# Optimization experiments

Hardware: AMD Instinct MI355X
Metric: run time of the kernel (lower is better)

The kernel has to match this reference:

```python
import jax, jax.numpy as jnp
import numpy as np

NSAMPLE = 64
RADIUS = 0.3
HMIN = -0.2
HMAX_LIST = (0.1, 0.2, 0.3, 0.4)
NUM_ANGLE = 12
NUM_DEPTH = 4
EPS = 1e-5


def setup_inputs() -> dict:
    key = jax.random.key(0)
    ks = jax.random.split(key, 32)
    rn = lambda i, s: jax.random.normal(ks[i], s, dtype=jnp.float32)
    ru = lambda i, s: jax.random.uniform(ks[i], s, dtype=jnp.float32)
    return {
        'seed_xyz': rn(0, (2, 1024, 3)),
        'pointcloud': rn(1, (2, 8192, 3)),
        'vp_rot': rn(2, (2, 1024, 3, 3)),
        'cw1': rn(3, (64, 3)), 'cbn1': ru(4, (4, 64)),
        'cw2': rn(5, (128, 64)), 'cbn2': ru(6, (4, 128)),
        'cw3': rn(7, (256, 128)), 'cbn3': ru(8, (4, 256)),
        'ow1': rn(9, (128, 256)), 'ob1': rn(10, (128,)), 'obn1': ru(11, (4, 128)),
        'ow2': rn(12, (128, 128)), 'ob2': rn(13, (128,)), 'obn2': ru(14, (4, 128)),
        'ow3': rn(15, (36, 128)), 'ob3': rn(16, (36,)),
        'tw1': rn(17, (128, 256)), 'tb1': rn(18, (128,)), 'tbn1': ru(19, (4, 128)),
        'tw2': rn(20, (128, 128)), 'tb2': rn(21, (128,)), 'tbn2': ru(22, (4, 128)),
        'tw3': rn(23, (12, 128)), 'tb3': rn(24, (12,)),
    }


def _bn_relu(y, bn):
    g, b, m, v = bn[0], bn[1], bn[2], bn[3]
    return jax.nn.relu(g * (y - m) * jax.lax.rsqrt(v + EPS) + b)


def _bn(y, bn):
    g, b, m, v = bn[0], bn[1], bn[2], bn[3]
    return g * (y - m) * jax.lax.rsqrt(v + EPS) + b


def _forward(seed_xyz, pointcloud, vp_rot, cw1, cbn1, cw2, cbn2, cw3, cbn3,
             ow1, ob1, obn1, ow2, ob2, obn2, ow3, ob3,
             tw1, tb1, tbn1, tw2, tb2, tbn2, tw3, tb3):
    B, ns, _ = seed_xyz.shape
    N = pointcloud.shape[1]
    # relative coords of every scene point w.r.t. every seed, rotated into the
    # grasp-view frame (cylinder axis = x after rotation): (B, ns, N, 3)
    rel = pointcloud[:, None, :, :] - seed_xyz[:, :, None, :]
    rot_rel = jnp.einsum('bsnc,bscd->bsnd', rel, vp_rot)
    ax = rot_rel[..., 0]
    r2 = rot_rel[..., 1] ** 2 + rot_rel[..., 2] ** 2
    pref = jnp.arange(N, dtype=jnp.float32) / N  # earlier index preferred (CUDA scan order)
    groups = []
    for hmax in HMAX_LIST:
        mask = (ax > HMIN) & (ax < hmax) & (r2 < RADIUS * RADIUS)
        score = mask.astype(jnp.float32) * 2.0 - pref
        _, idx = jax.lax.top_k(score, NSAMPLE)  # (B, ns, NSAMPLE), first valid idxs in order
        valid = jnp.take_along_axis(mask, idx, axis=-1)
        idx = jnp.where(valid, idx, idx[..., :1])  # fill slots with first found index
        g = jnp.take_along_axis(rot_rel, idx[..., None], axis=2)  # (B, ns, NSAMPLE, 3)
        groups.append(g)
    feat = jnp.stack(groups, axis=2)  # (B, ns, num_depth, NSAMPLE, 3)
    feat = feat.reshape(B, ns * NUM_DEPTH, NSAMPLE, 3)
    # SharedMLP [3,64,128,256], conv2d 1x1 (no bias) + BN + ReLU
    h = _bn_relu(feat @ cw1.T, cbn1)
    h = _bn_relu(h @ cw2.T, cbn2)
    h = _bn_relu(h @ cw3.T, cbn3)
    vp = jnp.max(h, axis=2)  # max-pool over nsample -> (B, ns*num_depth, 256)

    def head(w1, b1, bn1, w2, b2, bn2, w3, b3):
        x = _bn_relu(vp @ w1.T + b1, bn1)
        x = _bn_relu(x @ w2.T + b2, bn2)
        return x @ w3.T + b3

    op = head(ow1, ob1, obn1, ow2, ob2, obn2, ow3, ob3)     # (B, ns*D, 3*num_angle)
    tol = head(tw1, tb1, tbn1, tw2, tb2, tbn2, tw3, tb3)    # (B, ns*D, num_angle)
    out = jnp.concatenate([op, tol], axis=-1)               # score|angle_cls|width|tolerance
    out = out.reshape(B, ns, NUM_DEPTH, 4 * NUM_ANGLE).transpose(0, 3, 1, 2)
    return out  # (B, 4*num_angle, num_seed, num_depth)


def reference(seed_xyz, pointcloud, vp_rot, cw1, cbn1, cw2, cbn2, cw3, cbn3,
              ow1, ob1, obn1, ow2, ob2, obn2, ow3, ob3,
              tw1, tb1, tbn1, tw2, tb2, tbn2, tw3, tb3):
    return _forward(seed_xyz, pointcloud, vp_rot, cw1, cbn1, cw2, cbn2, cw3, cbn3,
                    ow1, ob1, obn1, ow2, ob2, obn2, ow3, ob3,
                    tw1, tb1, tbn1, tw2, tb2, tbn2, tw3, tb3)
```

## Files before the change

### kernel.cpp

```cpp
#include <hip/hip_runtime.h>
#include <hip/hip_bf16.h>

#define NB    2
#define NS    1024
#define NPTS  8192
#define NGROUP (NB*NS*4)

enum : int {
  OFF_BW2  = 256,
  OFF_W1Q  = 4352,
  OFF_B2   = 8448,
  OFF_BW3  = 8576,
  OFF_B3   = 41344,
  OFF_HB1  = 41600,
  OFF_HB1B = 74368,
  OFF_HB2  = 74624,
  OFF_HB2B = 107392,
  OFF_HB3  = 107648,
  OFF_HB3B = 115840,
  PREP_TOTAL = 189632,
  OFF_FEAT = 146688,
  OFF_VP   = 1719552,
  OFF_CNT  = 3816704,
  OFF_FLAG = 3824896,
};

struct Ptrs { const void* p[25]; };

typedef __attribute__((ext_vector_type(8))) short bf16x8;
typedef __attribute__((ext_vector_type(4))) float f32x4;

template<typename T> struct LD;
template<> struct LD<float> {
  static __device__ __forceinline__ float get(const void* p, int i){ return ((const float*)p)[i]; }
};
template<> struct LD<__hip_bfloat16> {
  static __device__ __forceinline__ float get(const void* p, int i){ return __bfloat162float(((const __hip_bfloat16*)p)[i]); }
};

template<typename T>
__device__ __forceinline__ float bnscale(const void* bn, int C, int c){
  float g = LD<T>::get(bn, c);
  float v = LD<T>::get(bn, 3*C + c);
  return g / sqrtf(v + 1e-5f);
}

__device__ __forceinline__ unsigned short f2bf(float v){
  __hip_bfloat16 hb = __float2bfloat16(v);
  return *reinterpret_cast<unsigned short*>(&hb);
}

__global__ __launch_bounds__(256) void detect_kernel(const void* w2, const void* w3, int* flag){
  __shared__ int f;
  int t = threadIdx.x;
  if (t == 0) f = 0;
  __syncthreads();
  int loc = 0;
  const unsigned short* a = (const unsigned short*)w2;
  for (int i = t; i < 8192; i += 256)  loc |= ((a[i] & 0x7F80) == 0x7F80);
  const unsigned short* b = (const unsigned short*)w3;
  for (int i = t; i < 32768; i += 256) loc |= ((b[i] & 0x7F80) == 0x7F80);
  if (loc) atomicOr(&f, 1);
  __syncthreads();
  if (t == 0) flag[0] = f;
}

template<typename T>
__global__ __launch_bounds__(256) void prep_kernel(Ptrs in, float* __restrict__ ws, int want){
  if (((const volatile int*)(ws + OFF_FLAG))[0] != want) return;
  int i = blockIdx.x*256 + threadIdx.x;
  if (i >= PREP_TOTAL) return;
  if (i < 256) { int c = i>>2, d = i&3; float s = bnscale<T>(in.p[4],64,c);
    float v = (d<3) ? LD<T>::get(in.p[3], c*3+d)*s
                    : LD<T>::get(in.p[4],64+c) - LD<T>::get(in.p[4],2*64+c)*s;
    ws[OFF_W1Q+i] = v; return; }
  i -= 256;
  if (i < 8192) {
    int j = i&7, f = i>>3, lane = f&63, kn = f>>6, kt = kn&1, nt = kn>>1;
    int n = nt*16 + (lane&15), k = kt*32 + ((lane>>4)<<3) + j;
    float s = bnscale<T>(in.p[6],128,n);
    ((unsigned short*)(ws + OFF_BW2))[i] = f2bf(LD<T>::get(in.p[5], n*64+k)*s); return; }
  i -= 8192;
  if (i < 32768) {
    int j = i&7, f = i>>3, lane = f&63, kn = f>>6, kt = kn&3, nt = kn>>2;
    int n = nt*16 + (lane&15), k = kt*32 + ((lane>>4)<<3) + j;
    float s = bnscale<T>(in.p[8],256,n);
    ((unsigned short*)(ws + OFF_BW3))[i] = f2bf(LD<T>::get(in.p[7], n*128+k)*s); return; }
  i -= 32768;
  if (i < 128) { float s = bnscale<T>(in.p[6],128,i);
    ws[OFF_B2+i] = LD<T>::get(in.p[6],128+i) - LD<T>::get(in.p[6],2*128+i)*s; return; }
  i -= 128;
  if (i < 256) { float s = bnscale<T>(in.p[8],256,i);
    ws[OFF_B3+i] = LD<T>::get(in.p[8],256+i) - LD<T>::get(in.p[8],2*256+i)*s; return; }
  i -= 256;
  if (i < 65536) {
    int j = i&7, f = i>>3, lane = f&63, kn = f>>6, kt = kn&7, nt = kn>>3;
    int n = nt*16 + (lane&15), k = kt*32 + ((lane>>4)<<3) + j;
    float v;
    if (n < 128) v = LD<T>::get(in.p[9],  n*256+k)       * bnscale<T>(in.p[11],128,n);
    else         v = LD<T>::get(in.p[17], (n-128)*256+k) * bnscale<T>(in.p[19],128,n-128);
    ((unsigned short*)(ws + OFF_HB1))[i] = f2bf(v); return; }
  i -= 65536;
  if (i < 256) { int n = i; float v;
    if (n < 128) { float s = bnscale<T>(in.p[11],128,n);
      v = (LD<T>::get(in.p[10],n) - LD<T>::get(in.p[11],2*128+n))*s + LD<T>::get(in.p[11],128+n); }
    else { int m = n-128; float s = bnscale<T>(in.p[19],128,m);
      v = (LD<T>::get(in.p[18],m) - LD<T>::get(in.p[19],2*128+m))*s + LD<T>::get(in.p[19],128+m); }
    ws[OFF_HB1B+n] = v; return; }
  i -= 256;
  if (i < 65536) {
    int j = i&7, f = i>>3, lane = f&63, kn = f>>6, kt = kn&7, nt = kn>>3;
    int n = nt*16 + (lane&15), k = kt*32 + ((lane>>4)<<3) + j;
    float v = 0.f;
    if (n < 128) { if (k < 128)  v = LD<T>::get(in.p[12], n*128+k)            * bnscale<T>(in.p[14],128,n); }
    else         { if (k >= 128) v = LD<T>::get(in.p[20], (n-128)*128+(k-128)) * bnscale<T>(in.p[22],128,n-128); }
    ((unsigned short*)(ws + OFF_HB2))[i] = f2bf(v); return; }
  i -= 65536;
  if (i < 256) { int n = i; float v;
    if (n < 128) { float s = bnscale<T>(in.p[14],128,n);
      v = (LD<T>::get(in.p[13],n) - LD<T>::get(in.p[14],2*128+n))*s + LD<T>::get(in.p[14],128+n); }
    else { int m = n-128; float s = bnscale<T>(in.p[22],128,m);
      v = (LD<T>::get(in.p[21],m) - LD<T>::get(in.p[22],2*128+m))*s + LD<T>::get(in.p[22],128+m); }
    ws[OFF_HB2B+n] = v; return; }
  i -= 256;
  if (i < 16384) {
    int j = i&7, f = i>>3, lane = f&63, kn = f>>6, kt = kn&7, nt = kn>>3;
    int n = nt*16 + (lane&15), k = kt*32 + ((lane>>4)<<3) + j;
    float v = 0.f;
    if (n < 36)      { if (k < 128)  v = LD<T>::get(in.p[15], n*128+k); }
    else if (n < 48) { if (k >= 128) v = LD<T>::get(in.p[23], (n-36)*128+(k-128)); }
    ((unsigned short*)(ws + OFF_HB3))[i] = f2bf(v); return; }
  i -= 16384;
  { int n = i; float v = 0.f;
    if (n < 36) v = LD<T>::get(in.p[16], n);
    else if (n < 48) v = LD<T>::get(in.p[24], n-36);
    ws[OFF_HB3B+n] = v; }
}

template<typename T>
__global__ __launch_bounds__(256) void group_kernel(
    const void* __restrict__ seed, const void* __restrict__ pc,
    const void* __restrict__ vr, float* __restrict__ ws, int want)
{
#pragma clang fp contract(off)
  if (((const volatile int*)(ws + OFF_FLAG))[0] != want) return;
  float* feat = ws + OFF_FEAT;
  int* cnt = (int*)(ws + OFF_CNT);
  __shared__ float rxs[256], rys[256], rzs[256];
  int bs = blockIdx.x;
  int b = bs >> 10;
  int t = threadIdx.x;
  int wave = t >> 6, lane = t & 63;
  float sx = LD<T>::get(seed, bs*3+0), sy = LD<T>::get(seed, bs*3+1), sz = LD<T>::get(seed, bs*3+2);
  float r00=LD<T>::get(vr,bs*9+0), r01=LD<T>::get(vr,bs*9+1), r02=LD<T>::get(vr,bs*9+2);
  float r10=LD<T>::get(vr,bs*9+3), r11=LD<T>::get(vr,bs*9+4), r12=LD<T>::get(vr,bs*9+5);
  float r20=LD<T>::get(vr,bs*9+6), r21=LD<T>::get(vr,bs*9+7), r22=LD<T>::get(vr,bs*9+8);
  const float hmaxs[4] = {0.1f, 0.2f, 0.3f, 0.4f};
  float hmax = hmaxs[wave];
  int g = bs*4 + wave;
  float* fout = feat + g*192;
  int base = b*(NPTS*3);
  int count = 0;
  float p0x=0.f, p0y=0.f, p0z=0.f;
  for (int c0 = 0; c0 < NPTS; c0 += 256) {
    __syncthreads();
    { int pi = base + (c0 + t)*3;
      float e0 = LD<T>::get(pc, pi+0) - sx;
      float e1 = LD<T>::get(pc, pi+1) - sy;
      float e2 = LD<T>::get(pc, pi+2) - sz;
      rxs[t] = e0*r00 + e1*r10 + e2*r20;
      rys[t] = e0*r01 + e1*r11 + e2*r21;
      rzs[t] = e0*r02 + e1*r12 + e2*r22; }
    __syncthreads();
    if (count < 64) {
      for (int sub = 0; sub < 4; ++sub) {
        int idx = sub*64 + lane;
        float rx = rxs[idx], ry = rys[idx], rz = rzs[idx];
        float r2 = ry*ry + rz*rz;
        bool m = (rx > -0.2f) && (rx < hmax) && (r2 < 0.09f);
        unsigned long long bal = __ballot(m);
        int rank = __popcll(bal & ((1ull << lane) - 1ull));
        int slot = count + rank;
        if (m && slot < 64) { fout[slot*3+0]=rx; fout[slot*3+1]=ry; fout[slot*3+2]=rz; }
        count += __popcll(bal);
      }
    }
    if (c0 == 0) { p0x = rxs[0]; p0y = rys[0]; p0z = rzs[0]; }
  }
  if (count == 0) {
    if (lane == 0) { fout[0]=p0x; fout[1]=p0y; fout[2]=p0z; }
    count = 1;
  }
  if (lane == 0) cnt[g] = (count > 64) ? 64 : count;
}

__global__ __launch_bounds__(256) void mlp_kernel(float* __restrict__ ws){
  __shared__ unsigned short h2s[2][64*136];
  __shared__ float w1q[4][256];
  const int t = threadIdx.x;
  const int wave = t >> 6, lane = t & 63;
  const int quad = lane >> 4, l15 = lane & 15;
  const int grp = wave >> 1, nhalf = wave & 1;
  const int g = blockIdx.x*2 + grp;
  for (int i = t; i < 1024; i += 256) w1q[i>>8][i&255] = ws[OFF_W1Q + (i&255)];
  const int V = ((const int*)(ws + OFF_CNT))[g];
  const float* feat = ws + OFF_FEAT + g*192;
  __syncthreads();
  bf16x8 a1[4][2];
  const float* wq = w1q[quad];
#pragma unroll
  for (int mt = 0; mt < 4; ++mt) {
    const int m = mt*16 + l15;
    const float x0 = feat[m*3+0], x1 = feat[m*3+1], x2 = feat[m*3+2];
#pragma unroll
    for (int kt = 0; kt < 2; ++kt) {
      const int c0 = kt*32 + quad*8;
#pragma unroll
      for (int j = 0; j < 8; ++j) {
        const float* w = wq + (c0+j)*4;
        a1[mt][kt][j] = (short)f2bf(fmaxf(w[3] + x0*w[0] + x1*w[1] + x2*w[2], 0.f));
      }
    }
  }
  unsigned short* h2 = h2s[grp];
  const bf16x8* BW2 = (const bf16x8*)(ws + OFF_BW2);
#pragma unroll
  for (int nt4 = 0; nt4 < 4; ++nt4) {
    const int nt = nhalf*4 + nt4;
    const int n = nt*16 + l15;
    const float bias = ws[OFF_B2 + n];
    f32x4 acc[4];
#pragma unroll
    for (int mt = 0; mt < 4; ++mt) acc[mt] = (f32x4){bias, bias, bias, bias};
#pragma unroll
    for (int kt = 0; kt < 2; ++kt) {
      const bf16x8 b = BW2[(nt*2+kt)*64 + lane];
#pragma unroll
      for (int mt = 0; mt < 4; ++mt)
        acc[mt] = __builtin_amdgcn_mfma_f32_16x16x32_bf16(a1[mt][kt], b, acc[mt], 0, 0, 0);
    }
#pragma unroll
    for (int mt = 0; mt < 4; ++mt)
#pragma unroll
      for (int jj = 0; jj < 4; ++jj) {
        const int m = mt*16 + quad*4 + jj;
        h2[m*136 + n] = f2bf(fmaxf(acc[mt][jj], 0.f));
      }
  }
  __syncthreads();
  bf16x8 a2[4][4];
#pragma unroll
  for (int mt = 0; mt < 4; ++mt)
#pragma unroll
    for (int kt = 0; kt < 4; ++kt)
      a2[mt][kt] = *(const bf16x8*)&h2[(mt*16 + l15)*136 + kt*32 + quad*8];
  const bf16x8* BW3 = (const bf16x8*)(ws + OFF_BW3);
  float vpv[8];
#pragma unroll
  for (int nt8 = 0; nt8 < 8; ++nt8) {
    const int nt = nhalf*8 + nt8;
    const int n = nt*16 + l15;
    const float bias = ws[OFF_B3 + n];
    f32x4 acc[4];
#pragma unroll
    for (int mt = 0; mt < 4; ++mt) acc[mt] = (f32x4){bias, bias, bias, bias};
#pragma unroll
    for (int kt = 0; kt < 4; ++kt) {
      const bf16x8 b = BW3[(nt*4+kt)*64 + lane];
#pragma unroll
      for (int mt = 0; mt < 4; ++mt)
        acc[mt] = __builtin_amdgcn_mfma_f32_16x16x32_bf16(a2[mt][kt], b, acc[mt], 0, 0, 0);
    }
    float mx = 0.f;
#pragma unroll
    for (int mt = 0; mt < 4; ++mt)
#pragma unroll
      for (int jj = 0; jj < 4; ++jj) {
        const int row = mt*16 + quad*4 + jj;
        const float v = fmaxf(acc[mt][jj], 0.f);
        mx = (row < V) ? fmaxf(mx, v) : mx;
      }
    mx = fmaxf(mx, __shfl_xor(mx, 16, 64));
    mx = fmaxf(mx, __shfl_xor(mx, 32, 64));
    vpv[nt8] = mx;
  }
  if (quad == 0) {
    float* vp = ws + OFF_VP + g*256 + nhalf*128;
#pragma unroll
    for (int nt8 = 0; nt8 < 8; ++nt8) vp[nt8*16 + l15] = vpv[nt8];
  }
}

#define YSTRIDE 264
template<typename OUT>
__global__ __launch_bounds__(256) void heads_kernel(float* __restrict__ ws, OUT* __restrict__ out, int want){
  if (((const volatile int*)(ws + OFF_FLAG))[0] != want) return;
  __shared__ unsigned short y[16*YSTRIDE];
  const int t = threadIdx.x;
  const int wave = t >> 6, lane = t & 63;
  const int quad = lane >> 4, l15 = lane & 15;
  const int r0 = blockIdx.x * 16;
  bf16x8 a[8];
  const float* vp = ws + OFF_VP + (r0 + l15)*256;
#pragma unroll
  for (int kt = 0; kt < 8; ++kt) {
    const float4* v4 = (const float4*)(vp + kt*32 + quad*8);
    float4 u0 = v4[0], u1 = v4[1];
    a[kt][0]=(short)f2bf(u0.x); a[kt][1]=(short)f2bf(u0.y); a[kt][2]=(short)f2bf(u0.z); a[kt][3]=(short)f2bf(u0.w);
    a[kt][4]=(short)f2bf(u1.x); a[kt][5]=(short)f2bf(u1.y); a[kt][6]=(short)f2bf(u1.z); a[kt][7]=(short)f2bf(u1.w);
  }
  const bf16x8* HB1 = (const bf16x8*)(ws + OFF_HB1);
#pragma unroll
  for (int nt4 = 0; nt4 < 4; ++nt4) {
    const int nt = wave*4 + nt4;
    const int n = nt*16 + l15;
    const float bias = ws[OFF_HB1B + n];
    f32x4 acc = (f32x4){bias, bias, bias, bias};
#pragma unroll
    for (int kt = 0; kt < 8; ++kt)
      acc = __builtin_amdgcn_mfma_f32_16x16x32_bf16(a[kt], HB1[(nt*8+kt)*64 + lane], acc, 0, 0, 0);
#pragma unroll
    for (int jj = 0; jj < 4; ++jj)
      y[(quad*4+jj)*YSTRIDE + n] = f2bf(fmaxf(acc[jj], 0.f));
  }
  __syncthreads();
#pragma unroll
  for (int kt = 0; kt < 8; ++kt)
    a[kt] = *(const bf16x8*)&y[l15*YSTRIDE + kt*32 + quad*8];
  __syncthreads();
  const bf16x8* HB2 = (const bf16x8*)(ws + OFF_HB2);
#pragma unroll
  for (int nt4 = 0; nt4 < 4; ++nt4) {
    const int nt = wave*4 + nt4;
    const int n = nt*16 + l15;
    const float bias = ws[OFF_HB2B + n];
    f32x4 acc = (f32x4){bias, bias, bias, bias};
#pragma unroll
    for (int kt = 0; kt < 8; ++kt)
      acc = __builtin_amdgcn_mfma_f32_16x16x32_bf16(a[kt], HB2[(nt*8+kt)*64 + lane], acc, 0, 0, 0);
#pragma unroll
    for (int jj = 0; jj < 4; ++jj)
      y[(quad*4+jj)*YSTRIDE + n] = f2bf(fmaxf(acc[jj], 0.f));
  }
  __syncthreads();
#pragma unroll
  for (int kt = 0; kt < 8; ++kt)
    a[kt] = *(const bf16x8*)&y[l15*YSTRIDE + kt*32 + quad*8];
  const bf16x8* HB3 = (const bf16x8*)(ws + OFF_HB3);
  {
    const int n = wave*16 + l15;
    const float bias = ws[OFF_HB3B + n];
    f32x4 acc = (f32x4){bias, bias, bias, bias};
#pragma unroll
    for (int kt = 0; kt < 8; ++kt)
      acc = __builtin_amdgcn_mfma_f32_16x16x32_bf16(a[kt], HB3[(wave*8+kt)*64 + lane], acc, 0, 0, 0);
    if (n < 48) {
#pragma unroll
      for (int jj = 0; jj < 4; ++jj) {
        const int gr = r0 + quad*4 + jj;
        const int b = gr >> 12, rem = gr & 4095, s = rem >> 2, d = rem & 3;
        out[((b*48 + n)*1024 + s)*4 + d] = (OUT)acc[jj];
      }
    }
  }
}

extern "C" void kernel_launch(void* const* d_in, const int* in_sizes, int n_in,
                              void* d_out, int out_size, void* d_ws, size_t ws_size,
                              hipStream_t stream) {
  float* ws = (float*)d_ws;
  Ptrs P;
  for (int i = 0; i < 25; ++i) P.p[i] = d_in[i];
  detect_kernel<<<1, 256, 0, stream>>>(d_in[5], d_in[7], (int*)(ws + OFF_FLAG));
  prep_kernel<__hip_bfloat16><<<(PREP_TOTAL+255)/256, 256, 0, stream>>>(P, ws, 0);
  prep_kernel<float><<<(PREP_TOTAL+255)/256, 256, 0, stream>>>(P, ws, 1);
  group_kernel<__hip_bfloat16><<<NB*NS, 256, 0, stream>>>(d_in[0], d_in[1], d_in[2], ws, 0);
  group_kernel<float><<<NB*NS, 256, 0, stream>>>(d_in[0], d_in[1], d_in[2], ws, 1);
  mlp_kernel<<<NGROUP/2, 256, 0, stream>>>(ws);
  heads_kernel<__hip_bfloat16><<<NGROUP/16, 256, 0, stream>>>(ws, (__hip_bfloat16*)d_out, 0);
  heads_kernel<float><<<NGROUP/16, 256, 0, stream>>>(ws, (float*)d_out, 1);
}
```

Before: 240.4 us.

## Double-buffer point staging, prefilter empty waves, skip empty MFMA row tiles

The grouping kernel now double-buffers the rotated point coordinates in shared memory, so staging the next chunk overlaps with scanning the current one and one barrier per iteration is removed. While staging, each wave also ballots a loose mask using the widest height bound, so scanning waves can skip 64-point sub-chunks that hold no candidates. The MLP kernel skips MFMA row tiles beyond the valid sample count, avoiding matrix work on padding rows. These add branches inside unrolled loops, which may raise register pressure or cause divergence-related code bloat, and the double buffer doubles the shared-memory footprint.

```diff
diff --git a/kernel.cpp b/kernel.cpp
--- a/kernel.cpp
+++ b/kernel.cpp
@@ -146,7 +146,8 @@
   if (((const volatile int*)(ws + OFF_FLAG))[0] != want) return;
   float* feat = ws + OFF_FEAT;
   int* cnt = (int*)(ws + OFF_CNT);
-  __shared__ float rxs[256], rys[256], rzs[256];
+  __shared__ float rxs[2][256], rys[2][256], rzs[2][256];
+  __shared__ unsigned long long loose[2][4];
   int bs = blockIdx.x;
   int b = bs >> 10;
   int t = threadIdx.x;
@@ -162,20 +163,34 @@
   int base = b*(NPTS*3);
   int count = 0;
   float p0x=0.f, p0y=0.f, p0z=0.f;
-  for (int c0 = 0; c0 < NPTS; c0 += 256) {
+
+  auto stage = [&](int c0, int buf){
+    int pi = base + (c0 + t)*3;
+    float e0 = LD<T>::get(pc, pi+0) - sx;
+    float e1 = LD<T>::get(pc, pi+1) - sy;
+    float e2 = LD<T>::get(pc, pi+2) - sz;
+    float rx = e0*r00 + e1*r10 + e2*r20;
+    float ry = e0*r01 + e1*r11 + e2*r21;
+    float rz = e0*r02 + e1*r12 + e2*r22;
+    rxs[buf][t] = rx; rys[buf][t] = ry; rzs[buf][t] = rz;
+    float r2 = ry*ry + rz*rz;
+    bool lm = (rx > -0.2f) && (rx < 0.4f) && (r2 < 0.09f);
+    unsigned long long bal = __ballot(lm);
+    if (lane == 0) loose[buf][wave] = bal;
+  };
+
+  stage(0, 0);
+  for (int c = 0; c < NPTS/256; ++c) {
+    int buf = c & 1;
     __syncthreads();
-    { int pi = base + (c0 + t)*3;
-      float e0 = LD<T>::get(pc, pi+0) - sx;
-      float e1 = LD<T>::get(pc, pi+1) - sy;
-      float e2 = LD<T>::get(pc, pi+2) - sz;
-      rxs[t] = e0*r00 + e1*r10 + e2*r20;
-      rys[t] = e0*r01 + e1*r11 + e2*r21;
-      rzs[t] = e0*r02 + e1*r12 + e2*r22; }
-    __syncthreads();
+    if (c == 0) { p0x = rxs[0][0]; p0y = rys[0][0]; p0z = rzs[0][0]; }
+    if (c + 1 < NPTS/256) stage((c+1)*256, 1 - buf);
     if (count < 64) {
       for (int sub = 0; sub < 4; ++sub) {
+        unsigned long long lb = loose[buf][sub];
+        if (lb == 0ull) continue;
         int idx = sub*64 + lane;
-        float rx = rxs[idx], ry = rys[idx], rz = rzs[idx];
+        float rx = rxs[buf][idx], ry = rys[buf][idx], rz = rzs[buf][idx];
         float r2 = ry*ry + rz*rz;
         bool m = (rx > -0.2f) && (rx < hmax) && (r2 < 0.09f);
         unsigned long long bal = __ballot(m);
@@ -185,7 +200,6 @@
         count += __popcll(bal);
       }
     }
-    if (c0 == 0) { p0x = rxs[0]; p0y = rys[0]; p0z = rzs[0]; }
   }
   if (count == 0) {
     if (lane == 0) { fout[0]=p0x; fout[1]=p0y; fout[2]=p0z; }
@@ -204,12 +218,13 @@
   const int g = blockIdx.x*2 + grp;
   for (int i = t; i < 1024; i += 256) w1q[i>>8][i&255] = ws[OFF_W1Q + (i&255)];
   const int V = ((const int*)(ws + OFF_CNT))[g];
+  const int MT = (V + 15) >> 4;
   const float* feat = ws + OFF_FEAT + g*192;
   __syncthreads();
   bf16x8 a1[4][2];
   const float* wq = w1q[quad];
 #pragma unroll
-  for (int mt = 0; mt < 4; ++mt) {
+  for (int mt = 0; mt < 4; ++mt) if (mt < MT) {
     const int m = mt*16 + l15;
     const float x0 = feat[m*3+0], x1 = feat[m*3+1], x2 = feat[m*3+2];
 #pragma unroll
@@ -231,16 +246,16 @@
     const float bias = ws[OFF_B2 + n];
     f32x4 acc[4];
 #pragma unroll
-    for (int mt = 0; mt < 4; ++mt) acc[mt] = (f32x4){bias, bias, bias, bias};
+    for (int mt = 0; mt < 4; ++mt) if (mt < MT) acc[mt] = (f32x4){bias, bias, bias, bias};
 #pragma unroll
     for (int kt = 0; kt < 2; ++kt) {
       const bf16x8 b = BW2[(nt*2+kt)*64 + lane];
 #pragma unroll
-      for (int mt = 0; mt < 4; ++mt)
+      for (int mt = 0; mt < 4; ++mt) if (mt < MT)
         acc[mt] = __builtin_amdgcn_mfma_f32_16x16x32_bf16(a1[mt][kt], b, acc[mt], 0, 0, 0);
     }
 #pragma unroll
-    for (int mt = 0; mt < 4; ++mt)
+    for (int mt = 0; mt < 4; ++mt) if (mt < MT)
 #pragma unroll
       for (int jj = 0; jj < 4; ++jj) {
         const int m = mt*16 + quad*4 + jj;
@@ -250,7 +265,7 @@
   __syncthreads();
   bf16x8 a2[4][4];
 #pragma unroll
-  for (int mt = 0; mt < 4; ++mt)
+  for (int mt = 0; mt < 4; ++mt) if (mt < MT)
 #pragma unroll
     for (int kt = 0; kt < 4; ++kt)
       a2[mt][kt] = *(const bf16x8*)&h2[(mt*16 + l15)*136 + kt*32 + quad*8];
@@ -263,17 +278,17 @@
     const float bias = ws[OFF_B3 + n];
     f32x4 acc[4];
 #pragma unroll
-    for (int mt = 0; mt < 4; ++mt) acc[mt] = (f32x4){bias, bias, bias, bias};
+    for (int mt = 0; mt < 4; ++mt) if (mt < MT) acc[mt] = (f32x4){bias, bias, bias, bias};
 #pragma unroll
     for (int kt = 0; kt < 4; ++kt) {
       const bf16x8 b = BW3[(nt*4+kt)*64 + lane];
 #pragma unroll
-      for (int mt = 0; mt < 4; ++mt)
+      for (int mt = 0; mt < 4; ++mt) if (mt < MT)
         acc[mt] = __builtin_amdgcn_mfma_f32_16x16x32_bf16(a2[mt][kt], b, acc[mt], 0, 0, 0);
     }
     float mx = 0.f;
 #pragma unroll
-    for (int mt = 0; mt < 4; ++mt)
+    for (int mt = 0; mt < 4; ++mt) if (mt < MT)
 #pragma unroll
       for (int jj = 0; jj < 4; ++jj) {
         const int row = mt*16 + quad*4 + jj;
```

Result: slower. 356.9 us (+48.5%).

## Restructure grouping to one wave per seed over all heights and merge dtype launches

Applied to the files above, without the earlier changes.

The grouping kernel now gives each wave a whole seed and classifies every point against all four height thresholds in one pass. Before, each block handled one seed, staged rotated points in shared memory, and used a wave per threshold. This removes the shared-memory staging and block barriers and computes each point's rotation once instead of four times. Waves can no longer stop early per threshold and must scan all 8192 points. The dtype-specific duplicate launches of prep, group and heads are merged into single launches that branch on the flag at runtime, cutting empty kernel launches.

```diff
diff --git a/kernel.cpp b/kernel.cpp
--- a/kernel.cpp
+++ b/kernel.cpp
@@ -66,10 +66,7 @@
 }
 
 template<typename T>
-__global__ __launch_bounds__(256) void prep_kernel(Ptrs in, float* __restrict__ ws, int want){
-  if (((const volatile int*)(ws + OFF_FLAG))[0] != want) return;
-  int i = blockIdx.x*256 + threadIdx.x;
-  if (i >= PREP_TOTAL) return;
+__device__ void prep_body(const Ptrs& in, float* __restrict__ ws, int i){
   if (i < 256) { int c = i>>2, d = i&3; float s = bnscale<T>(in.p[4],64,c);
     float v = (d<3) ? LD<T>::get(in.p[3], c*3+d)*s
                     : LD<T>::get(in.p[4],64+c) - LD<T>::get(in.p[4],2*64+c)*s;
@@ -137,61 +134,80 @@
     ws[OFF_HB3B+n] = v; }
 }
 
+__global__ __launch_bounds__(256) void prep_kernel(Ptrs in, float* __restrict__ ws){
+  int i = blockIdx.x*256 + threadIdx.x;
+  if (i >= PREP_TOTAL) return;
+  if (((const volatile int*)(ws + OFF_FLAG))[0]) prep_body<float>(in, ws, i);
+  else                                           prep_body<__hip_bfloat16>(in, ws, i);
+}
+
 template<typename T>
-__global__ __launch_bounds__(256) void group_kernel(
-    const void* __restrict__ seed, const void* __restrict__ pc,
-    const void* __restrict__ vr, float* __restrict__ ws, int want)
-{
+__device__ void group_body(const void* __restrict__ seed, const void* __restrict__ pc,
+                           float* __restrict__ ws, const void* __restrict__ vr, int bs){
 #pragma clang fp contract(off)
-  if (((const volatile int*)(ws + OFF_FLAG))[0] != want) return;
   float* feat = ws + OFF_FEAT;
   int* cnt = (int*)(ws + OFF_CNT);
-  __shared__ float rxs[256], rys[256], rzs[256];
-  int bs = blockIdx.x;
-  int b = bs >> 10;
-  int t = threadIdx.x;
-  int wave = t >> 6, lane = t & 63;
+  const int lane = threadIdx.x & 63;
+  const int b = bs >> 10;
   float sx = LD<T>::get(seed, bs*3+0), sy = LD<T>::get(seed, bs*3+1), sz = LD<T>::get(seed, bs*3+2);
   float r00=LD<T>::get(vr,bs*9+0), r01=LD<T>::get(vr,bs*9+1), r02=LD<T>::get(vr,bs*9+2);
   float r10=LD<T>::get(vr,bs*9+3), r11=LD<T>::get(vr,bs*9+4), r12=LD<T>::get(vr,bs*9+5);
   float r20=LD<T>::get(vr,bs*9+6), r21=LD<T>::get(vr,bs*9+7), r22=LD<T>::get(vr,bs*9+8);
-  const float hmaxs[4] = {0.1f, 0.2f, 0.3f, 0.4f};
-  float hmax = hmaxs[wave];
-  int g = bs*4 + wave;
-  float* fout = feat + g*192;
-  int base = b*(NPTS*3);
-  int count = 0;
+  float* f0 = feat + (bs*4+0)*192;
+  float* f1 = feat + (bs*4+1)*192;
+  float* f2 = feat + (bs*4+2)*192;
+  float* f3 = feat + (bs*4+3)*192;
+  int c0n=0, c1n=0, c2n=0, c3n=0;
+  const int base = b*(NPTS*3);
   float p0x=0.f, p0y=0.f, p0z=0.f;
-  for (int c0 = 0; c0 < NPTS; c0 += 256) {
-    __syncthreads();
-    { int pi = base + (c0 + t)*3;
-      float e0 = LD<T>::get(pc, pi+0) - sx;
-      float e1 = LD<T>::get(pc, pi+1) - sy;
-      float e2 = LD<T>::get(pc, pi+2) - sz;
-      rxs[t] = e0*r00 + e1*r10 + e2*r20;
-      rys[t] = e0*r01 + e1*r11 + e2*r21;
-      rzs[t] = e0*r02 + e1*r12 + e2*r22; }
-    __syncthreads();
-    if (count < 64) {
-      for (int sub = 0; sub < 4; ++sub) {
-        int idx = sub*64 + lane;
-        float rx = rxs[idx], ry = rys[idx], rz = rzs[idx];
-        float r2 = ry*ry + rz*rz;
-        bool m = (rx > -0.2f) && (rx < hmax) && (r2 < 0.09f);
-        unsigned long long bal = __ballot(m);
-        int rank = __popcll(bal & ((1ull << lane) - 1ull));
-        int slot = count + rank;
-        if (m && slot < 64) { fout[slot*3+0]=rx; fout[slot*3+1]=ry; fout[slot*3+2]=rz; }
-        count += __popcll(bal);
-      }
-    }
-    if (c0 == 0) { p0x = rxs[0]; p0y = rys[0]; p0z = rzs[0]; }
-  }
-  if (count == 0) {
-    if (lane == 0) { fout[0]=p0x; fout[1]=p0y; fout[2]=p0z; }
-    count = 1;
-  }
-  if (lane == 0) cnt[g] = (count > 64) ? 64 : count;
+  for (int c = 0; c < NPTS/64; ++c) {
+    const int pi = base + (c*64 + lane)*3;
+    float e0 = LD<T>::get(pc, pi+0) - sx;
+    float e1 = LD<T>::get(pc, pi+1) - sy;
+    float e2 = LD<T>::get(pc, pi+2) - sz;
+    float rx = e0*r00 + e1*r10 + e2*r20;
+    float ry = e0*r01 + e1*r11 + e2*r21;
+    float rz = e0*r02 + e1*r12 + e2*r22;
+    float r2 = ry*ry + rz*rz;
+    if (c == 0 && lane == 0) { p0x = rx; p0y = ry; p0z = rz; }
+    const bool mb = (rx > -0.2f) && (r2 < 0.09f);
+    const unsigned long long pm = (1ull << lane) - 1ull;
+    { bool m = mb && (rx < 0.1f); unsigned long long bal = __ballot(m);
+      if (bal) { int slot = c0n + __popcll(bal & pm);
+        if (m && slot < 64) { f0[slot*3]=rx; f0[slot*3+1]=ry; f0[slot*3+2]=rz; }
+        c0n += __popcll(bal); } }
+    { bool m = mb && (rx < 0.2f); unsigned long long bal = __ballot(m);
+      if (bal) { int slot = c1n + __popcll(bal & pm);
+        if (m && slot < 64) { f1[slot*3]=rx; f1[slot*3+1]=ry; f1[slot*3+2]=rz; }
+        c1n += __popcll(bal); } }
+    { bool m = mb && (rx < 0.3f); unsigned long long bal = __ballot(m);
+      if (bal) { int slot = c2n + __popcll(bal & pm);
+        if (m && slot < 64) { f2[slot*3]=rx; f2[slot*3+1]=ry; f2[slot*3+2]=rz; }
+        c2n += __popcll(bal); } }
+    { bool m = mb && (rx < 0.4f); unsigned long long bal = __ballot(m);
+      if (bal) { int slot = c3n + __popcll(bal & pm);
+        if (m && slot < 64) { f3[slot*3]=rx; f3[slot*3+1]=ry; f3[slot*3+2]=rz; }
+        c3n += __popcll(bal); } }
+  }
+  if (lane == 0) {
+    if (c0n == 0) { f0[0]=p0x; f0[1]=p0y; f0[2]=p0z; c0n = 1; }
+    if (c1n == 0) { f1[0]=p0x; f1[1]=p0y; f1[2]=p0z; c1n = 1; }
+    if (c2n == 0) { f2[0]=p0x; f2[1]=p0y; f2[2]=p0z; c2n = 1; }
+    if (c3n == 0) { f3[0]=p0x; f3[1]=p0y; f3[2]=p0z; c3n = 1; }
+    cnt[bs*4+0] = (c0n > 64) ? 64 : c0n;
+    cnt[bs*4+1] = (c1n > 64) ? 64 : c1n;
+    cnt[bs*4+2] = (c2n > 64) ? 64 : c2n;
+    cnt[bs*4+3] = (c3n > 64) ? 64 : c3n;
+  }
+}
+
+__global__ __launch_bounds__(256) void group_kernel(
+    const void* __restrict__ seed, const void* __restrict__ pc,
+    const void* __restrict__ vr, float* __restrict__ ws)
+{
+  const int bs = blockIdx.x*4 + (threadIdx.x >> 6);
+  if (((const volatile int*)(ws + OFF_FLAG))[0]) group_body<float>(seed, pc, ws, vr, bs);
+  else                                           group_body<__hip_bfloat16>(seed, pc, ws, vr, bs);
 }
 
 __global__ __launch_bounds__(256) void mlp_kernel(float* __restrict__ ws){
@@ -292,9 +308,8 @@
 }
 
 #define YSTRIDE 264
-template<typename OUT>
-__global__ __launch_bounds__(256) void heads_kernel(float* __restrict__ ws, OUT* __restrict__ out, int want){
-  if (((const volatile int*)(ws + OFF_FLAG))[0] != want) return;
+__global__ __launch_bounds__(256) void heads_kernel(float* __restrict__ ws, void* __restrict__ outv){
+  const int isf32 = ((const volatile int*)(ws + OFF_FLAG))[0];
   __shared__ unsigned short y[16*YSTRIDE];
   const int t = threadIdx.x;
   const int wave = t >> 6, lane = t & 63;
@@ -359,7 +374,9 @@
       for (int jj = 0; jj < 4; ++jj) {
         const int gr = r0 + quad*4 + jj;
         const int b = gr >> 12, rem = gr & 4095, s = rem >> 2, d = rem & 3;
-        out[((b*48 + n)*1024 + s)*4 + d] = (OUT)acc[jj];
+        const int o = ((b*48 + n)*1024 + s)*4 + d;
+        if (isf32) ((float*)outv)[o] = acc[jj];
+        else       ((__hip_bfloat16*)outv)[o] = __float2bfloat16(acc[jj]);
       }
     }
   }
@@ -372,11 +389,8 @@
   Ptrs P;
   for (int i = 0; i < 25; ++i) P.p[i] = d_in[i];
   detect_kernel<<<1, 256, 0, stream>>>(d_in[5], d_in[7], (int*)(ws + OFF_FLAG));
-  prep_kernel<__hip_bfloat16><<<(PREP_TOTAL+255)/256, 256, 0, stream>>>(P, ws, 0);
-  prep_kernel<float><<<(PREP_TOTAL+255)/256, 256, 0, stream>>>(P, ws, 1);
-  group_kernel<__hip_bfloat16><<<NB*NS, 256, 0, stream>>>(d_in[0], d_in[1], d_in[2], ws, 0);
-  group_kernel<float><<<NB*NS, 256, 0, stream>>>(d_in[0], d_in[1], d_in[2], ws, 1);
+  prep_kernel<<<(PREP_TOTAL+255)/256, 256, 0, stream>>>(P, ws);
+  group_kernel<<<NB*NS/4, 256, 0, stream>>>(d_in[0], d_in[1], d_in[2], ws);
   mlp_kernel<<<NGROUP/2, 256, 0, stream>>>(ws);
-  heads_kernel<__hip_bfloat16><<<NGROUP/16, 256, 0, stream>>>(ws, (__hip_bfloat16*)d_out, 0);
-  heads_kernel<float><<<NGROUP/16, 256, 0, stream>>>(ws, (float*)d_out, 1);
-}
+  heads_kernel<<<NGROUP/16, 256, 0, stream>>>(ws, d_out);
+}
```

Result: slower. 260.2 us (+8.2%).
